# Optimization experiments

Hardware: AMD Instinct MI355X
Metric: run time of the kernel (lower is better)

The kernel has to match this reference:

```python
import jax, jax.numpy as jnp
import numpy as np


def _sin_rpe(Lq, d_model, dtype):
    # sinusoidal relative-position embeddings for positions -(Lq-1)..(Lq-1)
    inv_freq = 1.0 / (10000.0 ** (jnp.arange(0, d_model, 2, dtype=jnp.float32) / d_model))
    pos = jnp.arange(-(Lq - 1), Lq, dtype=jnp.float32)  # [2Lq-1]
    ang = pos[:, None] * inv_freq[None, :]               # [2Lq-1, d_model/2]
    emb = jnp.zeros((2 * Lq - 1, d_model), dtype=jnp.float32)
    emb = emb.at[:, 0::2].set(jnp.sin(ang)).at[:, 1::2].set(jnp.cos(ang))
    return emb.astype(dtype)


def _rel_shift(x):
    # Transformer-XL relative shift. x: [B,H,Lq,Lr] with Lr = 2Lq-1
    B, H, Lq, Lr = x.shape
    xp = jnp.concatenate([jnp.zeros((B, H, Lq, 1), x.dtype), x], axis=-1)
    xp = xp.reshape(B, H, Lr + 1, Lq)
    return xp[:, :, 1:].reshape(B, H, Lq, Lr)[..., Lr - Lq:]


def setup_inputs() -> dict:
    key = jax.random.key(0)
    ks = jax.random.split(key, 7)
    B, Lq, D, H = 1, 2048, 1024, 16
    d_head = D // H
    s = 0.02
    return {
        "w": jax.random.normal(ks[0], (B, Lq, D), jnp.float32),
        "Wq": jax.random.normal(ks[1], (D, D), jnp.float32) * s,
        "Wk": jax.random.normal(ks[2], (D, D), jnp.float32) * s,
        "Wv": jax.random.normal(ks[3], (D, D), jnp.float32) * s,
        "Wr": jax.random.normal(ks[4], (D, D), jnp.float32) * s,
        "u_bias": jax.random.normal(ks[5], (H, d_head), jnp.float32) * 0.02,
        "v_bias": jax.random.normal(ks[6], (H, d_head), jnp.float32) * 0.02,
    }


def reference(w, Wq, Wk, Wv, Wr, u_bias, v_bias):
    B, Lq, D = w.shape
    H, d_head = u_bias.shape
    scale = 1.0 / np.sqrt(d_head).astype(np.float32)
    r = _sin_rpe(Lq, D, w.dtype)                          # [2Lq-1, D]
    # torch Linear: y = x @ W.T
    q = (w @ Wq.T).reshape(B, Lq, H, d_head).transpose(0, 2, 1, 3)  # [B,H,Lq,d]
    k = (w @ Wk.T).reshape(B, Lq, H, d_head).transpose(0, 2, 1, 3)
    v = (w @ Wv.T).reshape(B, Lq, H, d_head).transpose(0, 2, 1, 3)
    rp = (r @ Wr.T).reshape(2 * Lq - 1, H, d_head).transpose(1, 0, 2)  # [H,2Lq-1,d]
    AC = jnp.einsum('bhid,bhjd->bhij', q + u_bias[None, :, None, :], k)   # [B,H,Lq,Lq]
    BD = jnp.einsum('bhid,hjd->bhij', q + v_bias[None, :, None, :], rp)   # [B,H,Lq,2Lq-1]
    BD = _rel_shift(BD)                                                   # [B,H,Lq,Lq]
    attn = jax.nn.softmax((AC + BD) * scale, axis=-1)
    out = jnp.einsum('bhij,bhjd->bhid', attn, v)          # [B,H,Lq,d]
    return out.transpose(0, 2, 1, 3).reshape(B, Lq, D)
```

## Files before the change

### kernel.cpp

```cpp
#include <hip/hip_runtime.h>
#include <math.h>
#include <stddef.h>

#define LQ 2048
#define DM 1024
#define NH 16
#define DH 64
#define LR 4095

typedef __attribute__((ext_vector_type(4))) float f4v;
typedef __attribute__((ext_vector_type(8))) short s8v;
typedef __attribute__((ext_vector_type(2))) unsigned short us2;
typedef __attribute__((ext_vector_type(8))) unsigned short us8;
typedef __attribute__((ext_vector_type(2))) unsigned int u32x2;
typedef __attribute__((ext_vector_type(4))) unsigned int u32x4;

__device__ __forceinline__ unsigned short f2bf(float x) {
    unsigned int u = __float_as_uint(x);
    return (unsigned short)((u + 0x7FFFu + ((u >> 16) & 1u)) >> 16);
}
__device__ __forceinline__ float bf2f(unsigned short s) {
    return __uint_as_float(((unsigned int)s) << 16);
}
__device__ __forceinline__ unsigned cvtpk(float lo, float hi) {
    unsigned r;
    asm("v_cvt_pk_bf16_f32 %0, %1, %2" : "=v"(r) : "v"(lo), "v"(hi));
    return r;
}
template<int CTRL>
__device__ __forceinline__ float rot16(float x) {
    return __uint_as_float((unsigned)__builtin_amdgcn_update_dpp(
        0, (int)__float_as_uint(x), CTRL, 0xF, 0xF, false));
}
#define GLOAD16(g, l) __builtin_amdgcn_global_load_lds((g), (l), 16, 0, 0)
#define WAVE_LDS_FENCE() do { \
    asm volatile("s_waitcnt lgkmcnt(0)" ::: "memory"); \
    __builtin_amdgcn_sched_barrier(0); } while (0)

#define MFMA16(a, b, c) __builtin_amdgcn_mfma_f32_16x16x32_bf16((a), (b), (c), 0, 0, 0)

__device__ __forceinline__ s8v sw_read8(const unsigned short* base, int row, int colshort) {
    int byte = (row * 128 + colshort * 2) ^ ((row & 7) << 4);
    return *(const s8v*)((const char*)base + byte);
}

__global__ __launch_bounds__(256)
void prep(const float* __restrict__ w, const float* __restrict__ Wq,
          const float* __restrict__ Wk, const float* __restrict__ Wv,
          const float* __restrict__ Wr, unsigned short* __restrict__ dst,
          unsigned short* __restrict__ r, unsigned short* __restrict__ rpg) {
    int b = blockIdx.x;
    if (b < 3072) {
        size_t e0 = ((size_t)b * 256 + threadIdx.x) * 8;
        const float* src;
        if (e0 < (size_t)LQ * DM) src = w + e0;
        else {
            size_t ro = e0 - (size_t)LQ * DM;
            int wi = (int)(ro >> 20);
            size_t off = ro & 1048575;
            src = (wi == 0 ? Wq : wi == 1 ? Wk : wi == 2 ? Wv : Wr) + off;
        }
        f4v a = *(const f4v*)src;
        f4v c = *(const f4v*)(src + 4);
        us8 o;
        o[0]=f2bf(a[0]); o[1]=f2bf(a[1]); o[2]=f2bf(a[2]); o[3]=f2bf(a[3]);
        o[4]=f2bf(c[0]); o[5]=f2bf(c[1]); o[6]=f2bf(c[2]); o[7]=f2bf(c[3]);
        *(us8*)(dst + e0) = o;
    } else if (b < 11262) {
        int tg = (b - 3072) * 256 + threadIdx.x;
        int gm = tg >> 9, c2 = tg & 511;
        float invf = expf(-(float)c2 * (9.210340371976184f / 512.0f));
        float ang = (float)(gm - (LQ - 1)) * invf;
        float sv, cv;
        sincosf(ang, &sv, &cv);
        us2 o; o[0] = f2bf(sv); o[1] = f2bf(cv);
        *(us2*)&r[(size_t)gm * DM + c2 * 2] = o;
    } else {
        int idx = (b - 11262) * 2048 + threadIdx.x * 8;
        unsigned short* p = (idx < 131072)
            ? (rpg - 131072 + idx)
            : (rpg + (size_t)LR * DM + (idx - 131072));
        *(us8*)p = (us8){0,0,0,0,0,0,0,0};
    }
}

__global__ __launch_bounds__(256)
void proj_all(const unsigned short* __restrict__ wbf, const unsigned short* __restrict__ rr,
              const unsigned short* __restrict__ Wqb, const unsigned short* __restrict__ Wkb,
              const unsigned short* __restrict__ Wvb, const unsigned short* __restrict__ Wrb,
              unsigned short* __restrict__ qb, unsigned short* __restrict__ kkb,
              unsigned short* __restrict__ vtg, unsigned short* __restrict__ rpg) {
    __shared__ unsigned short ldsbuf[2 * 128 * 64];
    unsigned short* As = ldsbuf;
    unsigned short* Bs = ldsbuf + 128 * 64;
    int bid = (blockIdx.x & 7) * 80 + (blockIdx.x >> 3);
    int mat, mblk, nblk;
    if (bid < 384) { mat = bid >> 7; int rm = bid & 127; mblk = rm >> 3; nblk = rm & 7; }
    else           { mat = 3; int rm = bid - 384; mblk = rm >> 3; nblk = rm & 7; }
    const int M = (mat < 3) ? LQ : LR;
    const unsigned short* A = (mat < 3) ? wbf : rr;
    const unsigned short* B = mat == 0 ? Wqb : mat == 1 ? Wkb : mat == 2 ? Wvb : Wrb;
    unsigned short* C = mat == 0 ? qb : mat == 1 ? kkb : mat == 2 ? vtg : rpg;
    const int m0 = mblk * 128, n0 = nblk * 128;
    const int t = threadIdx.x;
    const int w = t >> 6, lan16 = t & 15, lgrp = (t & 63) >> 4;
    const int wm = (w >> 1) * 64, wn = (w & 1) * 64;
    f4v acc[4][4] = {};

    for (int k0 = 0; k0 < DM; k0 += 64) {
        #pragma unroll
        for (int it = 0; it < 4; ++it) {
            int slot = it * 256 + t;
            int row = slot >> 3, c8 = slot & 7;
            int gm = m0 + row; if (gm > M - 1) gm = M - 1;
            GLOAD16(A + (size_t)gm * DM + k0 + c8 * 8,
                    (char*)As + (size_t)(it * 256 + (t & ~63)) * 16);
            GLOAD16(B + (size_t)(n0 + row) * DM + k0 + c8 * 8,
                    (char*)Bs + (size_t)(it * 256 + (t & ~63)) * 16);
        }
        __syncthreads();
        #pragma unroll
        for (int kk = 0; kk < 2; ++kk) {
            s8v aF[4], bF[4];
            #pragma unroll
            for (int i = 0; i < 4; ++i) {
                aF[i] = *(const s8v*)&As[(wm + i * 16 + lan16) * 64 + kk * 32 + lgrp * 8];
                bF[i] = *(const s8v*)&Bs[(wn + i * 16 + lan16) * 64 + kk * 32 + lgrp * 8];
            }
            #pragma unroll
            for (int i = 0; i < 4; ++i)
                #pragma unroll
                for (int j = 0; j < 4; ++j)
                    acc[i][j] = MFMA16(aF[i], bF[j], acc[i][j]);
        }
        __syncthreads();
    }
    if (mat != 2) {
        #pragma unroll
        for (int i = 0; i < 4; ++i)
            #pragma unroll
            for (int j = 0; j < 4; ++j)
                #pragma unroll
                for (int rg = 0; rg < 4; ++rg) {
                    int row = m0 + wm + i * 16 + lgrp * 4 + rg;
                    if (row < M)
                        C[(size_t)row * DM + n0 + wn + j * 16 + lan16] = f2bf(acc[i][j][rg]);
                }
    } else {
        unsigned short* Ct = ldsbuf;
        #pragma unroll
        for (int i = 0; i < 4; ++i)
            #pragma unroll
            for (int j = 0; j < 4; ++j) {
                int n = wn + j * 16 + lan16;
                int mb = wm + i * 16 + lgrp * 4;
                int byte = (n * 256 + mb * 2) ^ ((n & 7) << 4);
                u32x2 pp;
                pp[0] = cvtpk(acc[i][j][0], acc[i][j][1]);
                pp[1] = cvtpk(acc[i][j][2], acc[i][j][3]);
                *(u32x2*)((char*)Ct + byte) = pp;
            }
        __syncthreads();
        #pragma unroll
        for (int it = 0; it < 8; ++it) {
            int slot = it * 256 + t;
            int n = slot >> 4, c8 = slot & 15;
            int byte = (n * 256 + c8 * 16) ^ ((n & 7) << 4);
            us8 v = *(const us8*)((const char*)Ct + byte);
            *(us8*)&C[(size_t)(n0 + n) * LQ + m0 + c8 * 8] = v;
        }
    }
}

__global__ __launch_bounds__(256, 2)
void attn_mfma(const unsigned short* __restrict__ q, const unsigned short* __restrict__ kkg,
               const unsigned short* __restrict__ vtg, const unsigned short* __restrict__ rpg,
               const float* __restrict__ ub, const float* __restrict__ vb,
               float* __restrict__ out) {
    __shared__ unsigned short Kb[2][64 * 64];
    __shared__ unsigned short Bb[2][128 * 64];
    __shared__ unsigned short Vb[64 * 64];
    __shared__ unsigned short Gtw[4][80 * 20];
    __shared__ unsigned short Pt[4][64 * 18];

    const int dd = blockIdx.x;
    const int f = (dd & 7) * 64 + (dd >> 3);
    const int h = f >> 5;
    const int i0 = (f & 31) * 64;
    const int col0 = h * DH;

    const int t = threadIdx.x;
    const int w = t >> 6, lan16 = t & 15, lgrp = (t & 63) >> 4;
    const int W = w * 16;
    const int cbase = 48 - W;
    const float C1 = 0.125f * 1.4426950408889634f;
    const float C0 = -4.0f * 1.4426950408889634f;

    unsigned short* gw = Gtw[w];
    unsigned short* pw = Pt[w];

    union uv { u32x4 u; s8v s; };
    auto mkfrag = [&](int gi, const float* bias, s8v* dstf) {
        #pragma unroll
        for (int kk = 0; kk < 2; ++kk) {
            int cb = kk * 32 + lgrp * 8;
            us8 qv = (us8){0,0,0,0,0,0,0,0};
            if (gi < LQ) qv = *(const us8*)(q + (size_t)gi * DM + col0 + cb);
            f4v b0 = *(const f4v*)(bias + col0 + cb);
            f4v b1 = *(const f4v*)(bias + col0 + cb + 4);
            uv o;
            o.u[0] = cvtpk(bf2f(qv[0]) + b0[0], bf2f(qv[1]) + b0[1]);
            o.u[1] = cvtpk(bf2f(qv[2]) + b0[2], bf2f(qv[3]) + b0[3]);
            o.u[2] = cvtpk(bf2f(qv[4]) + b1[0], bf2f(qv[5]) + b1[1]);
            o.u[3] = cvtpk(bf2f(qv[6]) + b1[2], bf2f(qv[7]) + b1[3]);
            dstf[kk] = o.s;
        }
    };
    s8v quF[2], qvlF[2], qvsF[2];
    mkfrag(i0 + W + lan16, ub, quF);
    mkfrag(i0 + W + lan16, vb, qvlF);
    mkfrag(i0 + W + 1 + lan16, vb, qvsF);

    auto stageK = [&](int j0, int buf) {
        #pragma unroll
        for (int it = 0; it < 2; ++it) {
            int slot = it * 256 + t;
            int row = slot >> 3, c8 = (t & 7) ^ (row & 7);
            GLOAD16(kkg + (size_t)(j0 + row) * DM + col0 + c8 * 8,
                    (char*)&Kb[buf][0] + (size_t)(it * 256 + (t & ~63)) * 16);
        }
    };
    auto stageB = [&](int rel, int buf) {
        int base = (rel <= 0) ? rel + 4031 : rel - 65;
        #pragma unroll
        for (int it = 0; it < 4; ++it) {
            int slot = it * 256 + t;
            int row = slot >> 3, c8 = (t & 7) ^ (row & 7);
            GLOAD16(rpg + (ptrdiff_t)(base + row) * DM + col0 + c8 * 8,
                    (char*)&Bb[buf][0] + (size_t)(it * 256 + (t & ~63)) * 16);
        }
    };
    auto stageV = [&](int j0) {
        #pragma unroll
        for (int it = 0; it < 2; ++it) {
            int slot = it * 256 + t;
            int row = slot >> 3, c8 = (t & 7) ^ (row & 7);
            GLOAD16(vtg + (size_t)(col0 + row) * LQ + j0 + c8 * 8,
                    (char*)&Vb[0] + (size_t)(it * 256 + (t & ~63)) * 16);
        }
    };

    f4v accO[4] = {};
    float lsum[4] = {0.f, 0.f, 0.f, 0.f};

    stageK(0, 0);
    stageB(0 - i0, 0);

    auto tile_body = [&](int tt, int cur) {
        const int j0 = tt * 64;
        const int rel = j0 - i0;
        stageV(j0);
        const int tn = (tt < 31) ? tt + 1 : 31;
        stageK(tn * 64, cur ^ 1);
        stageB(tn * 64 - i0, cur ^ 1);
        __builtin_amdgcn_sched_barrier(0);
        asm volatile("s_waitcnt vmcnt(8)" ::: "memory");
        __builtin_amdgcn_s_barrier();
        __builtin_amdgcn_sched_barrier(0);

        __builtin_amdgcn_s_setprio(1);
        f4v acF[4] = {};
        #pragma unroll
        for (int nf = 0; nf < 4; ++nf)
            #pragma unroll
            for (int kk = 0; kk < 2; ++kk) {
                s8v bF = sw_read8(&Kb[cur][0], nf * 16 + lan16, kk * 32 + lgrp * 8);
                acF[nf] = MFMA16(quF[kk], bF, acF[nf]);
            }
        f4v g[5] = {};
        {
            const s8v* qf = (rel <= 0) ? qvlF : qvsF;
            #pragma unroll
            for (int c = 0; c < 5; ++c)
                #pragma unroll
                for (int kk = 0; kk < 2; ++kk) {
                    s8v bF = sw_read8(&Bb[cur][0], cbase + c * 16 + lan16, kk * 32 + lgrp * 8);
                    g[c] = MFMA16(qf[kk], bF, g[c]);
                }
        }
        __builtin_amdgcn_s_setprio(0);
        if (rel == 0) {
            #pragma unroll
            for (int c = 0; c < 5; ++c) {
                int trow = -65 + cbase + c * 16 + lan16;
                const unsigned short* bp = rpg + (ptrdiff_t)trow * DM + col0;
                #pragma unroll
                for (int kk = 0; kk < 2; ++kk) {
                    us8 bv = *(const us8*)(bp + kk * 32 + lgrp * 8);
                    g[c] = MFMA16(qvsF[kk], (s8v)bv, g[c]);
                }
            }
        }
        #pragma unroll
        for (int c = 0; c < 5; ++c) {
            int cl = c * 16 + lan16;
            u32x2 pp;
            pp[0] = cvtpk(g[c][0], g[c][1]);
            pp[1] = cvtpk(g[c][2], g[c][3]);
            *(u32x2*)&gw[cl * 20 + lgrp * 4] = pp;
        }
        WAVE_LDS_FENCE();

        #pragma unroll
        for (int nf = 0; nf < 4; ++nf) {
            int jl = nf * 16 + lan16;
            float pp[4];
            #pragma unroll
            for (int rg = 0; rg < 4; ++rg) {
                const int rhat = lgrp * 4 + rg;
                float bd = bf2f(gw[(jl - rhat + 15) * 20 + rhat]);
                pp[rg] = exp2f(fmaf(acF[nf][rg] + bd, C1, C0));
                lsum[rg] += pp[rg];
            }
            *(unsigned*)&pw[jl * 18 + lgrp * 4]     = cvtpk(pp[0], pp[1]);
            *(unsigned*)&pw[jl * 18 + lgrp * 4 + 2] = cvtpk(pp[2], pp[3]);
        }
        WAVE_LDS_FENCE();

        s8v pF[2];
        #pragma unroll
        for (int kk = 0; kk < 2; ++kk) {
            us8 tmp;
            #pragma unroll
            for (int e = 0; e < 8; ++e)
                tmp[e] = pw[(kk * 32 + lgrp * 8 + e) * 18 + lan16];
            pF[kk] = (s8v)tmp;
        }
        __builtin_amdgcn_sched_barrier(0);
        asm volatile("s_waitcnt vmcnt(6)" ::: "memory");
        __builtin_amdgcn_s_barrier();
        __builtin_amdgcn_sched_barrier(0);

        __builtin_amdgcn_s_setprio(1);
        #pragma unroll
        for (int nf = 0; nf < 4; ++nf)
            #pragma unroll
            for (int kk = 0; kk < 2; ++kk) {
                s8v vF = sw_read8(&Vb[0], nf * 16 + lan16, kk * 32 + lgrp * 8);
                accO[nf] = MFMA16(pF[kk], vF, accO[nf]);
            }
        __builtin_amdgcn_s_setprio(0);
        __builtin_amdgcn_sched_barrier(0);
        __builtin_amdgcn_s_barrier();
        __builtin_amdgcn_sched_barrier(0);
    };

    #pragma unroll 1
    for (int tp = 0; tp < 16; ++tp) {
        tile_body(tp * 2, 0);
        tile_body(tp * 2 + 1, 1);
    }

    #pragma unroll
    for (int rg = 0; rg < 4; ++rg) {
        float s = lsum[rg];
        s += rot16<0x121>(s);
        s += rot16<0x122>(s);
        s += rot16<0x124>(s);
        s += rot16<0x128>(s);
        float inv = 1.f / s;
        const int row = i0 + W + lgrp * 4 + rg;
        #pragma unroll
        for (int nf = 0; nf < 4; ++nf)
            out[(size_t)row * DM + col0 + nf * 16 + lan16] = accO[nf][rg] * inv;
    }
}

extern "C" void kernel_launch(void* const* d_in, const int* in_sizes, int n_in,
                              void* d_out, int out_size, void* d_ws, size_t ws_size,
                              hipStream_t stream) {
    const float* w  = (const float*)d_in[0];
    const float* Wq = (const float*)d_in[1];
    const float* Wk = (const float*)d_in[2];
    const float* Wv = (const float*)d_in[3];
    const float* Wr = (const float*)d_in[4];
    const float* ub = (const float*)d_in[5];
    const float* vb = (const float*)d_in[6];
    float* out = (float*)d_out;

    const size_t U = 1048576;
    unsigned short* ws = (unsigned short*)d_ws;
    unsigned short* wbf = ws;
    unsigned short* Wqb = ws + 2 * U;
    unsigned short* Wkb = ws + 3 * U;
    unsigned short* Wvb = ws + 4 * U;
    unsigned short* Wrb = ws + 5 * U;
    unsigned short* qb  = ws + 6 * U;
    unsigned short* kkb = ws + 8 * U;
    unsigned short* vtg = ws + 10 * U;
    unsigned short* rpg = ws + 12 * U + 131072;
    unsigned short* r   = rpg + (size_t)LR * DM + 131072;

    dim3 blk(256);
    hipLaunchKernelGGL(prep, dim3(11390), blk, 0, stream, w, Wq, Wk, Wv, Wr, wbf, r, rpg);
    hipLaunchKernelGGL(proj_all, dim3(640), blk, 0, stream,
                       wbf, r, Wqb, Wkb, Wvb, Wrb, qb, kkb, vtg, rpg);
    hipLaunchKernelGGL(attn_mfma, dim3(512), blk, 0, stream,
                       qb, kkb, vtg, rpg, ub, vb, out);
}
```

Measured before the change: 132.4 us.

## Software-pipeline PV matmul one tile behind and double-buffer V in attention

Restructures the attention tile loop so the P·V MFMA for the previous tile runs at the start of the next iteration. V is double-buffered, and K/B prefetch moves two tiles ahead, issued after the end-of-tile barrier. This removes one block barrier and one vmcnt wait per tile and overlaps the PV matmul with the QK/QR loads. The per-wave G and P scratch buffers are merged into one to save LDS. The projection kernel's block-index swizzle is also dropped. The deeper pipeline adds register pressure and changes the vmcnt accounting, which risks stalls or ordering mistakes.

```diff
diff --git a/kernel.cpp b/kernel.cpp
--- a/kernel.cpp
+++ b/kernel.cpp
@@ -93,7 +93,7 @@
     __shared__ unsigned short ldsbuf[2 * 128 * 64];
     unsigned short* As = ldsbuf;
     unsigned short* Bs = ldsbuf + 128 * 64;
-    int bid = (blockIdx.x & 7) * 80 + (blockIdx.x >> 3);
+    int bid = blockIdx.x;
     int mat, mblk, nblk;
     if (bid < 384) { mat = bid >> 7; int rm = bid & 127; mblk = rm >> 3; nblk = rm & 7; }
     else           { mat = 3; int rm = bid - 384; mblk = rm >> 3; nblk = rm & 7; }
@@ -179,9 +179,8 @@
                float* __restrict__ out) {
     __shared__ unsigned short Kb[2][64 * 64];
     __shared__ unsigned short Bb[2][128 * 64];
-    __shared__ unsigned short Vb[64 * 64];
-    __shared__ unsigned short Gtw[4][80 * 20];
-    __shared__ unsigned short Pt[4][64 * 18];
+    __shared__ unsigned short Vb[2][64 * 64];
+    __shared__ unsigned short GP[4][80 * 20];
 
     const int dd = blockIdx.x;
     const int f = (dd & 7) * 64 + (dd >> 3);
@@ -196,8 +195,7 @@
     const float C1 = 0.125f * 1.4426950408889634f;
     const float C0 = -4.0f * 1.4426950408889634f;
 
-    unsigned short* gw = Gtw[w];
-    unsigned short* pw = Pt[w];
+    unsigned short* gw = GP[w];
 
     union uv { u32x4 u; s8v s; };
     auto mkfrag = [&](int gi, const float* bias, s8v* dstf) {
@@ -240,35 +238,43 @@
                     (char*)&Bb[buf][0] + (size_t)(it * 256 + (t & ~63)) * 16);
         }
     };
-    auto stageV = [&](int j0) {
+    auto stageV = [&](int j0, int buf) {
         #pragma unroll
         for (int it = 0; it < 2; ++it) {
             int slot = it * 256 + t;
             int row = slot >> 3, c8 = (t & 7) ^ (row & 7);
             GLOAD16(vtg + (size_t)(col0 + row) * LQ + j0 + c8 * 8,
-                    (char*)&Vb[0] + (size_t)(it * 256 + (t & ~63)) * 16);
+                    (char*)&Vb[buf][0] + (size_t)(it * 256 + (t & ~63)) * 16);
         }
     };
 
     f4v accO[4] = {};
     float lsum[4] = {0.f, 0.f, 0.f, 0.f};
+    s8v pFprev[2] = {};
 
     stageK(0, 0);
     stageB(0 - i0, 0);
+    stageV(0, 1);
+    stageV(0, 0);
+    stageK(64, 1);
+    stageB(64 - i0, 1);
 
     auto tile_body = [&](int tt, int cur) {
         const int j0 = tt * 64;
         const int rel = j0 - i0;
-        stageV(j0);
-        const int tn = (tt < 31) ? tt + 1 : 31;
-        stageK(tn * 64, cur ^ 1);
-        stageB(tn * 64 - i0, cur ^ 1);
         __builtin_amdgcn_sched_barrier(0);
         asm volatile("s_waitcnt vmcnt(8)" ::: "memory");
         __builtin_amdgcn_s_barrier();
         __builtin_amdgcn_sched_barrier(0);
 
         __builtin_amdgcn_s_setprio(1);
+        #pragma unroll
+        for (int nf = 0; nf < 4; ++nf)
+            #pragma unroll
+            for (int kk = 0; kk < 2; ++kk) {
+                s8v vF = sw_read8(&Vb[cur ^ 1][0], nf * 16 + lan16, kk * 32 + lgrp * 8);
+                accO[nf] = MFMA16(pFprev[kk], vF, accO[nf]);
+            }
         f4v acF[4] = {};
         #pragma unroll
         for (int nf = 0; nf < 4; ++nf)
@@ -311,47 +317,48 @@
         }
         WAVE_LDS_FENCE();
 
+        float gval[16];
+        #pragma unroll
+        for (int nf = 0; nf < 4; ++nf)
+            #pragma unroll
+            for (int rg = 0; rg < 4; ++rg) {
+                const int rhat = lgrp * 4 + rg;
+                gval[nf * 4 + rg] = bf2f(gw[(nf * 16 + lan16 - rhat + 15) * 20 + rhat]);
+            }
+        WAVE_LDS_FENCE();
+
         #pragma unroll
         for (int nf = 0; nf < 4; ++nf) {
             int jl = nf * 16 + lan16;
             float pp[4];
             #pragma unroll
             for (int rg = 0; rg < 4; ++rg) {
-                const int rhat = lgrp * 4 + rg;
-                float bd = bf2f(gw[(jl - rhat + 15) * 20 + rhat]);
-                pp[rg] = exp2f(fmaf(acF[nf][rg] + bd, C1, C0));
+                pp[rg] = exp2f(fmaf(acF[nf][rg] + gval[nf * 4 + rg], C1, C0));
                 lsum[rg] += pp[rg];
             }
-            *(unsigned*)&pw[jl * 18 + lgrp * 4]     = cvtpk(pp[0], pp[1]);
-            *(unsigned*)&pw[jl * 18 + lgrp * 4 + 2] = cvtpk(pp[2], pp[3]);
+            u32x2 pk;
+            pk[0] = cvtpk(pp[0], pp[1]);
+            pk[1] = cvtpk(pp[2], pp[3]);
+            *(u32x2*)&gw[jl * 20 + lgrp * 4] = pk;
         }
         WAVE_LDS_FENCE();
 
-        s8v pF[2];
         #pragma unroll
         for (int kk = 0; kk < 2; ++kk) {
             us8 tmp;
             #pragma unroll
             for (int e = 0; e < 8; ++e)
-                tmp[e] = pw[(kk * 32 + lgrp * 8 + e) * 18 + lan16];
-            pF[kk] = (s8v)tmp;
+                tmp[e] = gw[(kk * 32 + lgrp * 8 + e) * 20 + lan16];
+            pFprev[kk] = (s8v)tmp;
         }
         __builtin_amdgcn_sched_barrier(0);
-        asm volatile("s_waitcnt vmcnt(6)" ::: "memory");
         __builtin_amdgcn_s_barrier();
         __builtin_amdgcn_sched_barrier(0);
-
-        __builtin_amdgcn_s_setprio(1);
-        #pragma unroll
-        for (int nf = 0; nf < 4; ++nf)
-            #pragma unroll
-            for (int kk = 0; kk < 2; ++kk) {
-                s8v vF = sw_read8(&Vb[0], nf * 16 + lan16, kk * 32 + lgrp * 8);
-                accO[nf] = MFMA16(pF[kk], vF, accO[nf]);
-            }
-        __builtin_amdgcn_s_setprio(0);
-        __builtin_amdgcn_sched_barrier(0);
-        __builtin_amdgcn_s_barrier();
+        const int tv = (tt < 31) ? tt + 1 : 31;
+        const int tn = (tt < 30) ? tt + 2 : 31;
+        stageV(tv * 64, cur ^ 1);
+        stageK(tn * 64, cur);
+        stageB(tn * 64 - i0, cur);
         __builtin_amdgcn_sched_barrier(0);
     };
 
@@ -360,6 +367,14 @@
         tile_body(tp * 2, 0);
         tile_body(tp * 2 + 1, 1);
     }
+
+    #pragma unroll
+    for (int nf = 0; nf < 4; ++nf)
+        #pragma unroll
+        for (int kk = 0; kk < 2; ++kk) {
+            s8v vF = sw_read8(&Vb[1][0], nf * 16 + lan16, kk * 32 + lgrp * 8);
+            accO[nf] = MFMA16(pFprev[kk], vF, accO[nf]);
+        }
 
     #pragma unroll
     for (int rg = 0; rg < 4; ++rg) {
```

After: 131.1 us. Within noise of the previous version (-1.0%).
